# Kernel tuning notes

Measured on AMD Instinct MI355X. Metric: run time of the kernel, lower is better.

The kernel has to match this reference:

```python
import jax, jax.numpy as jnp
import numpy as np

H = 2048      # num_hidden
B = 2048      # batch_size
T = 64        # seq_length
C = 10        # num_classes


def setup_inputs() -> dict:
    key = jax.random.key(0)
    k = jax.random.split(key, 4)
    bound = float(np.sqrt(1.0 / H))  # uniform(-bound, bound) init as in the torch module
    return {
        "x": jax.random.normal(k[0], (B, T), dtype=jnp.float32),
        "W_hx": jax.random.uniform(k[1], (H, 1), jnp.float32, -bound, bound),
        "W_hh": jax.random.uniform(k[2], (H, H), jnp.float32, -bound, bound),
        "W_hy": jax.random.uniform(k[3], (H, C), jnp.float32, -bound, bound),
        "b_h": jnp.zeros((H, 1), jnp.float32),
        "b_p": jnp.zeros((C, 1), jnp.float32),
    }


def reference(x, W_hx, W_hh, W_hy, b_h, b_p):
    # x: [B, T]; hidden state kept as [H, B] to match the torch layout.
    xT = x.T  # [T, B] so scan iterates over time

    def step(h, xt):
        # W_hx @ x_t  : [H,1] @ [1,B] -> [H,B]; W_hh @ h : [H,B]
        h = jnp.tanh(W_hx @ xt[None, :] + W_hh @ h + b_h)
        return h, None

    h0 = jnp.zeros((W_hh.shape[0], x.shape[0]), x.dtype)
    hT, _ = jax.lax.scan(step, h0, xT)
    out = W_hy.T @ hT + b_p  # [C, B]
    return out.T             # [B, C]
```

## Files before the change

### kernel.cpp

```cpp
#include <hip/hip_runtime.h>
#include <cstdint>
#include <cstddef>
#include <cmath>

#define H  2048
#define BB 2048
#define TT 64
#define NC 10

typedef __bf16 bf16;
typedef bf16  bf16x8 __attribute__((ext_vector_type(8)));
typedef float f32x4  __attribute__((ext_vector_type(4)));

__device__ __forceinline__ void load_lds16(const void* g, void* l) {
    __builtin_amdgcn_global_load_lds(
        (__attribute__((address_space(1))) void*)(void*)g,
        (__attribute__((address_space(3))) void*)l,
        16, 0, 0);
}

__global__ void w_shuffle_kernel(const float* __restrict__ Whh,
                                 bf16* __restrict__ Wshuf) {
    int tid = blockIdx.x * blockDim.x + threadIdx.x;
    int sub = tid >> 6;
    int l   = tid & 63;
    int n16 = sub >> 6;
    int k32 = sub & 63;
    int n = n16 * 16 + (l & 15);
    int k = k32 * 32 + (l >> 4) * 8;
    const float* src = Whh + (size_t)n * H + k;
    bf16x8 o;
#pragma unroll
    for (int j = 0; j < 8; ++j) o[j] = (bf16)src[j];
    *(bf16x8*)(Wshuf + (size_t)tid * 8) = o;
}

__global__ void rnn_init(const float* __restrict__ x,
                         const float* __restrict__ Whx,
                         const float* __restrict__ bh,
                         bf16* __restrict__ S) {
    int b  = blockIdx.x;
    int i0 = threadIdx.x * 8;
    float xv = x[(size_t)b * TT];
    bf16x8 o;
#pragma unroll
    for (int j = 0; j < 8; ++j)
        o[j] = (bf16)tanhf(Whx[i0 + j] * xv + bh[i0 + j]);
    size_t sub  = (size_t)(b >> 4) * 64 + (i0 >> 5);
    size_t slot = (size_t)(b & 15) | (size_t)(((i0 >> 3) & 3) << 4);
    *(bf16x8*)(S + (sub * 64 + slot) * 8) = o;
}

#define PH_WAIT(NSTR) asm volatile("s_waitcnt vmcnt(" NSTR ")" ::: "memory")
#define SBAR0()       __builtin_amdgcn_sched_barrier(0)

__launch_bounds__(512, 2)
__global__ void rnn_step(const float* __restrict__ x,
                         const float* __restrict__ Whx,
                         const float* __restrict__ bh,
                         const bf16*  __restrict__ Wshuf,
                         const bf16*  __restrict__ Sr,
                         bf16* __restrict__ Sw,
                         int t) {
    __shared__ __align__(16) char Bs[4][16384];

    const int tid  = threadIdx.x;
    const int w    = tid >> 6;
    const int lane = tid & 63;
    const int lrow = lane & 15;
    const int quad = lane >> 4;

    const int xcd = blockIdx.x & 7;
    const int loc = blockIdx.x >> 3;
    const int bm0 = (xcd * 2 + (loc & 1)) * 128;
    const int bn0 = (loc >> 1) * 128;

    const int qm   = w & 3;
    const int qn   = w >> 2;
    const int m16w = (bm0 >> 4) + qm * 2;
    const int cn0  = bn0 + qn * 64;
    const int n16b = bn0 >> 4;

    const bf16* pA  = Sr + (size_t)lane * 8;
    const bf16* pSt = Wshuf + ((size_t)(n16b + w) * 64) * 512 + (size_t)lane * 8;

    f32x4 acc[2][4];
#pragma unroll
    for (int i = 0; i < 2; ++i)
#pragma unroll
        for (int j = 0; j < 4; ++j) acc[i][j] = (f32x4){0.f, 0.f, 0.f, 0.f};

    bf16x8 Ar[4][2][2];

#define ISSUE(RI, pp)                                                        \
    {                                                                        \
        _Pragma("unroll")                                                    \
        for (int j = 0; j < 2; ++j) {                                        \
            load_lds16(pSt + (size_t)(2 * (pp) + j) * 512,                   \
                       &Bs[RI][(j * 8 + w) * 1024]);                         \
            _Pragma("unroll")                                                \
            for (int fm = 0; fm < 2; ++fm)                                   \
                Ar[RI][j][fm] = *(const bf16x8*)(pA +                        \
                    (size_t)((m16w + fm) * 64 + 2 * (pp) + j) * 512);        \
        }                                                                    \
    }

#define COMPUTE(RI)                                                          \
    {                                                                        \
        _Pragma("unroll")                                                    \
        for (int j = 0; j < 2; ++j) {                                        \
            bf16x8 Bf[4];                                                    \
            _Pragma("unroll")                                                \
            for (int fn = 0; fn < 4; ++fn)                                   \
                Bf[fn] = *(const bf16x8*)&Bs[RI]                             \
                    [(j * 8 + qn * 4 + fn) * 1024 + lane * 16];              \
            _Pragma("unroll")                                                \
            for (int fm = 0; fm < 2; ++fm)                                   \
                _Pragma("unroll")                                            \
                for (int fn = 0; fn < 4; ++fn)                               \
                    acc[fm][fn] = __builtin_amdgcn_mfma_f32_16x16x32_bf16(   \
                        Ar[RI][j][fm], Bf[fn], acc[fm][fn], 0, 0, 0);        \
        }                                                                    \
    }

#define PHASE(RI, RN, p, WNSTR, DOISS)                                       \
    {                                                                        \
        PH_WAIT(WNSTR);                                                      \
        SBAR0();                                                             \
        __builtin_amdgcn_s_barrier();                                        \
        SBAR0();                                                             \
        if (DOISS) ISSUE(RN, (p) + 3);                                       \
        SBAR0();                                                             \
        COMPUTE(RI);                                                         \
    }

    ISSUE(0, 0); SBAR0();
    ISSUE(1, 1); SBAR0();
    ISSUE(2, 2); SBAR0();

#pragma unroll 1
    for (int q = 0; q < 7; ++q) {
        int p = 4 * q;
        PHASE(0, 3, p + 0, "12", true);
        PHASE(1, 0, p + 1, "12", true);
        PHASE(2, 1, p + 2, "12", true);
        PHASE(3, 2, p + 3, "12", true);
    }
    PHASE(0, 3, 28, "12", true);
    PHASE(1, 0, 29, "12", false);
    PHASE(2, 1, 30, "6",  false);
    PHASE(3, 2, 31, "0",  false);

#undef PHASE
#undef COMPUTE
#undef ISSUE

    bf16* Lw = (bf16*)&Bs[0][0] + (size_t)w * 2048;
#pragma unroll
    for (int fm = 0; fm < 2; ++fm) {
        int rb = bm0 + qm * 32 + fm * 16 + quad * 4;
        float xv[4];
#pragma unroll
        for (int r = 0; r < 4; ++r) xv[r] = x[(size_t)(rb + r) * TT + t];
#pragma unroll
        for (int fn = 0; fn < 4; ++fn) {
            int col = cn0 + fn * 16 + lrow;
            float wx = Whx[col], bb = bh[col];
            int cbyte = (fn * 16 + lrow) * 2;
#pragma unroll
            for (int r = 0; r < 4; ++r) {
                int row_l = fm * 16 + quad * 4 + r;
                float z = acc[fm][fn][r] + wx * xv[r] + bb;
                *(bf16*)((char*)Lw + row_l * 128 +
                         (cbyte ^ ((row_l & 7) << 4))) = (bf16)tanhf(z);
            }
        }
    }
    __syncthreads();
#pragma unroll
    for (int fm = 0; fm < 2; ++fm) {
#pragma unroll
        for (int kc = 0; kc < 2; ++kc) {
            int row_l = fm * 16 + lrow;
            int cb    = (kc * 64 + quad * 16) ^ ((row_l & 7) << 4);
            bf16x8 v = *(const bf16x8*)((const char*)Lw + row_l * 128 + cb);
            size_t sub = (size_t)(m16w + fm) * 64 + (cn0 >> 5) + kc;
            *(bf16x8*)(Sw + (sub * 64 + lane) * 8) = v;
        }
    }
}

__global__ void out_proj(const bf16* __restrict__ S,
                         const float* __restrict__ Why,
                         const float* __restrict__ bp,
                         float* __restrict__ out) {
    int b = blockIdx.x, tid = threadIdx.x;
    int h0 = tid * 8;
    size_t sub  = (size_t)(b >> 4) * 64 + (h0 >> 5);
    size_t slot = (size_t)(b & 15) | (size_t)(((h0 >> 3) & 3) << 4);
    bf16x8 v = *(const bf16x8*)(S + (sub * 64 + slot) * 8);
    float p[NC];
#pragma unroll
    for (int c = 0; c < NC; ++c) p[c] = 0.f;
#pragma unroll
    for (int j = 0; j < 8; ++j) {
        float s = (float)v[j];
        const float* wr = Why + (size_t)(h0 + j) * NC;
#pragma unroll
        for (int c = 0; c < NC; ++c) p[c] += s * wr[c];
    }
    __shared__ float red[256 * NC];
#pragma unroll
    for (int c = 0; c < NC; ++c) red[tid * NC + c] = p[c];
    __syncthreads();
    for (int s = 128; s > 0; s >>= 1) {
        if (tid < s)
#pragma unroll
            for (int c = 0; c < NC; ++c) red[tid * NC + c] += red[(tid + s) * NC + c];
        __syncthreads();
    }
    if (tid < NC) out[(size_t)b * NC + tid] = red[tid] + bp[tid];
}

extern "C" void kernel_launch(void* const* d_in, const int* in_sizes, int n_in,
                              void* d_out, int out_size, void* d_ws, size_t ws_size,
                              hipStream_t stream) {
    const float* x   = (const float*)d_in[0];
    const float* Whx = (const float*)d_in[1];
    const float* Whh = (const float*)d_in[2];
    const float* Why = (const float*)d_in[3];
    const float* bh  = (const float*)d_in[4];
    const float* bp  = (const float*)d_in[5];
    float* out = (float*)d_out;

    bf16* Wshuf = (bf16*)d_ws;
    bf16* S0 = (bf16*)((char*)d_ws + (size_t)8 * 1024 * 1024);
    bf16* S1 = (bf16*)((char*)d_ws + (size_t)16 * 1024 * 1024);

    hipLaunchKernelGGL(w_shuffle_kernel, dim3((H * H / 8) / 256), dim3(256),
                       0, stream, Whh, Wshuf);

    hipLaunchKernelGGL(rnn_init, dim3(BB), dim3(256), 0, stream, x, Whx, bh, S1);

    for (int t = 1; t < TT; ++t) {
        const bf16* Srd = (t & 1) ? S1 : S0;
        bf16*       Swr = (t & 1) ? S0 : S1;
        hipLaunchKernelGGL(rnn_step, dim3(256), dim3(512), 0, stream,
                           x, Whx, bh, Wshuf, Srd, Swr, t);
    }

    hipLaunchKernelGGL(out_proj, dim3(BB), dim3(256), 0, stream, S0, Why, bp, out);
}
```

Baseline: 1.646 ms.

## Stage both A and B tiles through LDS and remap blocks for weight reuse

The activation operand A, previously loaded from global straight into registers, now goes through LDS via global_load_lds alongside the weight tiles, and the vmcnt wait counts are adjusted to match. The block-to-XCD mapping is swapped so each XCD covers a contiguous range of weight columns, which should improve L2 reuse of W_hh. MFMA sections are also wrapped in s_setprio. LDS use doubles to 128KB and the occupancy hint of 2 is dropped, so at most one block fits per CU, leaving less room to hide latency.

```diff
diff --git a/kernel.cpp b/kernel.cpp
--- a/kernel.cpp
+++ b/kernel.cpp
@@ -54,7 +54,7 @@
 #define PH_WAIT(NSTR) asm volatile("s_waitcnt vmcnt(" NSTR ")" ::: "memory")
 #define SBAR0()       __builtin_amdgcn_sched_barrier(0)
 
-__launch_bounds__(512, 2)
+__launch_bounds__(512)
 __global__ void rnn_step(const float* __restrict__ x,
                          const float* __restrict__ Whx,
                          const float* __restrict__ bh,
@@ -62,7 +62,7 @@
                          const bf16*  __restrict__ Sr,
                          bf16* __restrict__ Sw,
                          int t) {
-    __shared__ __align__(16) char Bs[4][16384];
+    __shared__ __align__(16) char Ls[4][32768];
 
     const int tid  = threadIdx.x;
     const int w    = tid >> 6;
@@ -72,36 +72,33 @@
 
     const int xcd = blockIdx.x & 7;
     const int loc = blockIdx.x >> 3;
-    const int bm0 = (xcd * 2 + (loc & 1)) * 128;
-    const int bn0 = (loc >> 1) * 128;
+    const int bm0 = (loc >> 1) * 128;
+    const int bn0 = xcd * 256 + (loc & 1) * 128;
 
     const int qm   = w & 3;
     const int qn   = w >> 2;
     const int m16w = (bm0 >> 4) + qm * 2;
     const int cn0  = bn0 + qn * 64;
-    const int n16b = bn0 >> 4;
-
-    const bf16* pA  = Sr + (size_t)lane * 8;
-    const bf16* pSt = Wshuf + ((size_t)(n16b + w) * 64) * 512 + (size_t)lane * 8;
+
+    const char* srcA = (const char*)Sr +
+        ((size_t)((bm0 >> 4) + w) * 64) * 1024 + (size_t)lane * 16;
+    const char* srcB = (const char*)Wshuf +
+        ((size_t)((bn0 >> 4) + w) * 64) * 1024 + (size_t)lane * 16;
 
     f32x4 acc[2][4];
 #pragma unroll
     for (int i = 0; i < 2; ++i)
 #pragma unroll
         for (int j = 0; j < 4; ++j) acc[i][j] = (f32x4){0.f, 0.f, 0.f, 0.f};
-
-    bf16x8 Ar[4][2][2];
 
 #define ISSUE(RI, pp)                                                        \
     {                                                                        \
         _Pragma("unroll")                                                    \
         for (int j = 0; j < 2; ++j) {                                        \
-            load_lds16(pSt + (size_t)(2 * (pp) + j) * 512,                   \
-                       &Bs[RI][(j * 8 + w) * 1024]);                         \
-            _Pragma("unroll")                                                \
-            for (int fm = 0; fm < 2; ++fm)                                   \
-                Ar[RI][j][fm] = *(const bf16x8*)(pA +                        \
-                    (size_t)((m16w + fm) * 64 + 2 * (pp) + j) * 512);        \
+            load_lds16(srcA + (size_t)(2 * (pp) + j) * 1024,                 \
+                       &Ls[RI][(j * 16 + w) * 1024]);                        \
+            load_lds16(srcB + (size_t)(2 * (pp) + j) * 1024,                 \
+                       &Ls[RI][(j * 16 + 8 + w) * 1024]);                    \
         }                                                                    \
     }
 
@@ -109,17 +106,23 @@
     {                                                                        \
         _Pragma("unroll")                                                    \
         for (int j = 0; j < 2; ++j) {                                        \
-            bf16x8 Bf[4];                                                    \
+            bf16x8 Af[2], Bf[4];                                             \
+            _Pragma("unroll")                                                \
+            for (int fm = 0; fm < 2; ++fm)                                   \
+                Af[fm] = *(const bf16x8*)&Ls[RI]                             \
+                    [(j * 16 + qm * 2 + fm) * 1024 + lane * 16];             \
             _Pragma("unroll")                                                \
             for (int fn = 0; fn < 4; ++fn)                                   \
-                Bf[fn] = *(const bf16x8*)&Bs[RI]                             \
-                    [(j * 8 + qn * 4 + fn) * 1024 + lane * 16];              \
+                Bf[fn] = *(const bf16x8*)&Ls[RI]                             \
+                    [(j * 16 + 8 + qn * 4 + fn) * 1024 + lane * 16];         \
+            __builtin_amdgcn_s_setprio(1);                                   \
             _Pragma("unroll")                                                \
             for (int fm = 0; fm < 2; ++fm)                                   \
                 _Pragma("unroll")                                            \
                 for (int fn = 0; fn < 4; ++fn)                               \
                     acc[fm][fn] = __builtin_amdgcn_mfma_f32_16x16x32_bf16(   \
-                        Ar[RI][j][fm], Bf[fn], acc[fm][fn], 0, 0, 0);        \
+                        Af[fm], Bf[fn], acc[fm][fn], 0, 0, 0);               \
+            __builtin_amdgcn_s_setprio(0);                                   \
         }                                                                    \
     }
 
@@ -141,21 +144,21 @@
 #pragma unroll 1
     for (int q = 0; q < 7; ++q) {
         int p = 4 * q;
-        PHASE(0, 3, p + 0, "12", true);
-        PHASE(1, 0, p + 1, "12", true);
-        PHASE(2, 1, p + 2, "12", true);
-        PHASE(3, 2, p + 3, "12", true);
-    }
-    PHASE(0, 3, 28, "12", true);
-    PHASE(1, 0, 29, "12", false);
-    PHASE(2, 1, 30, "6",  false);
-    PHASE(3, 2, 31, "0",  false);
+        PHASE(0, 3, p + 0, "8", true);
+        PHASE(1, 0, p + 1, "8", true);
+        PHASE(2, 1, p + 2, "8", true);
+        PHASE(3, 2, p + 3, "8", true);
+    }
+    PHASE(0, 3, 28, "8", true);
+    PHASE(1, 0, 29, "8", false);
+    PHASE(2, 1, 30, "4", false);
+    PHASE(3, 2, 31, "0", false);
 
 #undef PHASE
 #undef COMPUTE
 #undef ISSUE
 
-    bf16* Lw = (bf16*)&Bs[0][0] + (size_t)w * 2048;
+    bf16* Lw = (bf16*)&Ls[0][0] + (size_t)w * 2048;
 #pragma unroll
     for (int fm = 0; fm < 2; ++fm) {
         int rb = bm0 + qm * 32 + fm * 16 + quad * 4;
```

New measurement: 1.544 ms. 1.07x faster.
